# Kernel tuning notes

Hardware: AMD Instinct MI355X
Metric: run time of the kernel (lower is better)

The kernel has to match this reference:

```python
import jax, jax.numpy as jnp
import numpy as np
from jax import lax

WINDOW_SIZE = 11
SIGMA = 1.5
C1 = 0.01 ** 2
C2 = 0.03 ** 2


def _gaussian_window(channels: int) -> jnp.ndarray:
    x = np.arange(WINDOW_SIZE)
    g = np.exp(-((x - WINDOW_SIZE // 2) ** 2) / (2.0 * SIGMA ** 2))
    g = g / g.sum()
    w2d = np.outer(g, g).astype(np.float32)  # [k,k]
    # depthwise kernel: [C, 1, k, k] in OIHW with feature_group_count=C
    return jnp.asarray(np.tile(w2d[None, None], (channels, 1, 1, 1)))


def _depthwise_blur(x: jnp.ndarray, window: jnp.ndarray) -> jnp.ndarray:
    pad = WINDOW_SIZE // 2
    return lax.conv_general_dilated(
        x, window,
        window_strides=(1, 1),
        padding=[(pad, pad), (pad, pad)],
        feature_group_count=x.shape[1],
        dimension_numbers=("NCHW", "OIHW", "NCHW"),
    )


def setup_inputs() -> dict:
    key = jax.random.key(0)
    k1, k2 = jax.random.split(key)
    pred = jax.random.normal(k1, (16, 3, 512, 512), dtype=jnp.float32)
    target = jax.random.normal(k2, (16, 3, 512, 512), dtype=jnp.float32)
    return {"pred": pred, "target": target}


def reference(pred, target):
    pred = (pred + 1.0) / 2.0
    target = (target + 1.0) / 2.0
    channels = pred.shape[1]
    window = _gaussian_window(channels)

    mu_p = _depthwise_blur(pred, window)
    mu_t = _depthwise_blur(target, window)
    mu_p_sq = mu_p * mu_p
    mu_t_sq = mu_t * mu_t
    mu_pt = mu_p * mu_t

    sigma_p_sq = _depthwise_blur(pred * pred, window) - mu_p_sq
    sigma_t_sq = _depthwise_blur(target * target, window) - mu_t_sq
    sigma_pt = _depthwise_blur(pred * target, window) - mu_pt

    ssim_map = ((2.0 * mu_pt + C1) * (2.0 * sigma_pt + C2)) / (
        (mu_p_sq + mu_t_sq + C1) * (sigma_p_sq + sigma_t_sq + C2)
    )
    return 1.0 - jnp.mean(ssim_map)
```

## Files before the change

kernel.cpp:

```cpp
#include <hip/hip_runtime.h>
#include <math.h>


#define IMG 512
#define TW 64
#define TH 16
#define GXD 8
#define GYD 32
#define GZD 48
#define NB (GXD * GYD * GZD)
#define NB4 (NB * 4)
#define VBS 88
#define C1c 0.0001f
#define C2c 0.0009f
#define NTOTAL 12582912.0f
#define WS_NEED (1024 + (size_t)NB4 * 4)

typedef short bf16x8 __attribute__((ext_vector_type(8)));
typedef float f32x4 __attribute__((ext_vector_type(4)));
typedef float f32x2 __attribute__((ext_vector_type(2)));

struct GaussB { unsigned short gb[11]; };

__device__ __forceinline__ unsigned int pkbf(float a, float b) {
    return __builtin_amdgcn_perm(__float_as_uint(b), __float_as_uint(a),
                                 0x07060302u);
}


__device__ __forceinline__ void load_px(const float* __restrict__ pbase,
                                        const float* __restrict__ tbase,
                                        int gx, bool xin, int gy0,
                                        float (&pv)[8], float (&tv)[8]) {
    const bool ok = xin & (gy0 >= 0) & (gy0 <= IMG - 8);
    if (ok) {
        const float* pp = pbase + gy0 * IMG + gx;
        const float* tp = tbase + gy0 * IMG + gx;
        #pragma unroll
        for (int j = 0; j < 8; ++j) {
            pv[j] = pp[j * IMG];
            tv[j] = tp[j * IMG];
        }
    } else {
        #pragma unroll
        for (int j = 0; j < 8; ++j) {
            int gy = gy0 + j;
            bool in = xin && ((unsigned)gy < (unsigned)IMG);
            int idx = in ? (gy * IMG + gx) : 0;
            float a = pbase[idx];
            float b = tbase[idx];
            pv[j] = in ? a : 0.0f;
            tv[j] = in ? b : 0.0f;
        }
    }
}

__device__ __forceinline__ void pass_v_body(
    const float (&pv)[8], const float (&tv)[8], bf16x8 wfrag,
    unsigned short (*vb)[16][VBS], int n16, int vcol) {
    const f32x4 z = {0.0f, 0.0f, 0.0f, 0.0f};
    const f32x2 halfv = {0.5f, 0.5f};
    f32x2 p2[4], t2[4];
    #pragma unroll
    for (int h = 0; h < 4; ++h) {
        f32x2 pr = {pv[2*h], pv[2*h+1]};
        f32x2 tr = {tv[2*h], tv[2*h+1]};
        p2[h] = pr * halfv + halfv;
        t2[h] = tr * halfv + halfv;
    }
    #pragma unroll
    for (int ch = 0; ch < 5; ++ch) {
        union { bf16x8 v; unsigned int u[4]; } f;
        #pragma unroll
        for (int h = 0; h < 4; ++h) {
            f32x2 q;
            if      (ch == 0) q = p2[h];
            else if (ch == 1) q = t2[h];
            else if (ch == 2) q = p2[h] * p2[h];
            else if (ch == 3) q = t2[h] * t2[h];
            else              q = p2[h] * t2[h];
            f.u[h] = pkbf(q.x, q.y);
        }
        f32x4 d = __builtin_amdgcn_mfma_f32_16x16x32_bf16(f.v, wfrag, z, 0, 0, 0);
        union { ushort4 s; unsigned int u[2]; } pk;
        pk.u[0] = pkbf(d[0], d[1]);
        pk.u[1] = pkbf(d[2], d[3]);
        *(ushort4*)&vb[ch][n16][vcol] = pk.s;
    }
}

__device__ __forceinline__ float pass_h_body(
    unsigned short (*vb)[16][VBS], bf16x8 wfrag, int n16, int quad, int w) {
    const f32x4 z = {0.0f, 0.0f, 0.0f, 0.0f};
    float lsum = 0.0f;
    f32x4 r[5];
    #pragma unroll
    for (int ch = 0; ch < 5; ++ch) {
        bf16x8 a = *(const bf16x8*)&vb[ch][n16][16 * w + 8 * quad];
        r[ch] = __builtin_amdgcn_mfma_f32_16x16x32_bf16(a, wfrag, z, 0, 0, 0);
    }
    const f32x2 twov = {2.0f, 2.0f};
    const f32x2 c1v  = {C1c, C1c};
    const f32x2 c2v  = {C2c, C2c};
    #pragma unroll
    for (int jj = 0; jj < 2; ++jj) {
        f32x2 mp  = {r[0][2*jj], r[0][2*jj+1]};
        f32x2 mt  = {r[1][2*jj], r[1][2*jj+1]};
        f32x2 epp = {r[2][2*jj], r[2][2*jj+1]};
        f32x2 ett = {r[3][2*jj], r[3][2*jj+1]};
        f32x2 ept = {r[4][2*jj], r[4][2*jj+1]};
        f32x2 mp2 = mp * mp;
        f32x2 mt2 = mt * mt;
        f32x2 mpt = mp * mt;
        f32x2 sp_ = epp - mp2;
        f32x2 st_ = ett - mt2;
        f32x2 spt = ept - mpt;
        f32x2 num = (mpt * twov + c1v) * (spt * twov + c2v);
        f32x2 den = (mp2 + mt2 + c1v) * (sp_ + st_ + c2v);
        lsum = fmaf(num.x, __builtin_amdgcn_rcpf(den.x), lsum);
        lsum = fmaf(num.y, __builtin_amdgcn_rcpf(den.y), lsum);
    }
    return lsum;
}


__global__ __launch_bounds__(320, 6) void ssim_main_ws(
    const float* __restrict__ pred,
    const float* __restrict__ target,
    const unsigned short* __restrict__ wtab,
    float* __restrict__ partials)
{
    __shared__ unsigned short vb[5][16][VBS];

    const int tid  = threadIdx.x;
    const int w    = tid >> 6;
    const int lane = tid & 63;
    const int quad = lane >> 4;
    const int n16  = lane & 15;
    const int tx0  = blockIdx.x * TW;
    const int ty0  = blockIdx.y * TH;
    const float* __restrict__ pbase = pred   + (size_t)blockIdx.z * (IMG * IMG);
    const float* __restrict__ tbase = target + (size_t)blockIdx.z * (IMG * IMG);

    const int gx   = tx0 - 5 + 16 * w + n16;
    const bool xin = (unsigned)gx < (unsigned)IMG;
    const int gy0  = ty0 - 5 + quad * 8;
    const int vcol = 16 * w + 4 * quad;

    const bf16x8 wfrag = *(const bf16x8*)(wtab + n16 * 32 + quad * 8);

    float pv[8], tv[8];
    load_px(pbase, tbase, gx, xin, gy0, pv, tv);

    pass_v_body(pv, tv, wfrag, vb, n16, vcol);
    __syncthreads();

    float lsum = 0.0f;
    if (w < 4)
        lsum = pass_h_body(vb, wfrag, n16, quad, w);

    #pragma unroll
    for (int off = 32; off > 0; off >>= 1)
        lsum += __shfl_down(lsum, off, 64);
    if (lane == 0 && w < 4) {
        int bid = blockIdx.x + GXD * (blockIdx.y + GYD * blockIdx.z);
        partials[bid * 4 + w] = lsum;
    }
}


__global__ __launch_bounds__(320, 6) void ssim_main_atomic(
    const float* __restrict__ pred,
    const float* __restrict__ target,
    float* __restrict__ sink,
    GaussB gwb)
{
    __shared__ unsigned short Wmat[16][32];
    __shared__ unsigned short vb[5][16][VBS];
    __shared__ float red[5];

    const int tid  = threadIdx.x;
    const int w    = tid >> 6;
    const int lane = tid & 63;
    const int quad = lane >> 4;
    const int n16  = lane & 15;
    const int tx0  = blockIdx.x * TW;
    const int ty0  = blockIdx.y * TH;
    const float* __restrict__ pbase = pred   + (size_t)blockIdx.z * (IMG * IMG);
    const float* __restrict__ tbase = target + (size_t)blockIdx.z * (IMG * IMG);

    const int gx   = tx0 - 5 + 16 * w + n16;
    const bool xin = (unsigned)gx < (unsigned)IMG;
    const int gy0  = ty0 - 5 + quad * 8;
    const int vcol = 16 * w + 4 * quad;

    float pv[8], tv[8];
    load_px(pbase, tbase, gx, xin, gy0, pv, tv);

    for (int idx = tid; idx < 512; idx += 320) {
        int i = idx >> 5, k = idx & 31, d = k - i;
        Wmat[i][k] = (d >= 0 && d <= 10) ? gwb.gb[d] : 0;
    }
    __syncthreads();
    const bf16x8 wfrag = *(const bf16x8*)&Wmat[n16][quad * 8];

    pass_v_body(pv, tv, wfrag, vb, n16, vcol);
    __syncthreads();

    float lsum = 0.0f;
    if (w < 4)
        lsum = pass_h_body(vb, wfrag, n16, quad, w);

    #pragma unroll
    for (int off = 32; off > 0; off >>= 1)
        lsum += __shfl_down(lsum, off, 64);
    if (lane == 0) red[w] = lsum;
    __syncthreads();
    if (tid == 0)
        atomicAdd(sink, red[0] + red[1] + red[2] + red[3]);
}


__global__ __launch_bounds__(1024) void ssim_reduce(const float* __restrict__ partials,
                                                    float* __restrict__ out)
{
    __shared__ float red[16];
    const int tid = threadIdx.x;
    float s = 0.0f;
    const float4* p4 = (const float4*)partials;
    #pragma unroll
    for (int j = 0; j < NB4 / 4096; ++j) {
        float4 v = p4[tid + 1024 * j];
        s += v.x + v.y + v.z + v.w;
    }
    #pragma unroll
    for (int off = 32; off > 0; off >>= 1)
        s += __shfl_down(s, off, 64);
    if ((tid & 63) == 0) red[tid >> 6] = s;
    __syncthreads();
    if (tid == 0) {
        float t = 0.0f;
        #pragma unroll
        for (int k = 0; k < 16; ++k) t += red[k];
        out[0] = 1.0f - t / NTOTAL;
    }
}

__global__ void ssim_zero(float* accum) { accum[0] = 0.0f; }
__global__ void ssim_final(const float* accum, float* out) {
    out[0] = 1.0f - accum[0] / NTOTAL;
}


static unsigned short g_hostW[512];

extern "C" void kernel_launch(void* const* d_in, const int* in_sizes, int n_in,
                              void* d_out, int out_size, void* d_ws, size_t ws_size,
                              hipStream_t stream) {
    const float* pred   = (const float*)d_in[0];
    const float* target = (const float*)d_in[1];
    float* out = (float*)d_out;

    GaussB gwb;
    double vals[11], s = 0.0;
    for (int i = 0; i < 11; ++i) {
        double d = (double)i - 5.0;
        vals[i] = exp(-(d * d) / (2.0 * 1.5 * 1.5));
        s += vals[i];
    }
    for (int i = 0; i < 11; ++i) {
        float f = (float)(vals[i] / s);
        unsigned int u;
        __builtin_memcpy(&u, &f, 4);
        unsigned int rounded = (u + 0x7FFFu + ((u >> 16) & 1u)) >> 16;
        gwb.gb[i] = (unsigned short)rounded;
    }
    for (int i = 0; i < 16; ++i)
        for (int k = 0; k < 32; ++k) {
            int d = k - i;
            g_hostW[i * 32 + k] = (d >= 0 && d <= 10) ? gwb.gb[d] : 0;
        }

    dim3 grid(GXD, GYD, GZD);
    if (ws_size >= WS_NEED) {
        unsigned short* wtab = (unsigned short*)d_ws;
        float* partials = (float*)((char*)d_ws + 1024);
        hipMemcpyAsync(wtab, g_hostW, sizeof(g_hostW),
                       hipMemcpyHostToDevice, stream);
        ssim_main_ws<<<grid, 320, 0, stream>>>(pred, target, wtab, partials);
        ssim_reduce<<<1, 1024, 0, stream>>>(partials, out);
    } else {
        float* accum = (float*)d_ws;
        ssim_zero<<<1, 1, 0, stream>>>(accum);
        ssim_main_atomic<<<grid, 320, 0, stream>>>(pred, target, accum, gwb);
        ssim_final<<<1, 1, 0, stream>>>(accum, out);
    }
}
```

Baseline: 137.6 us.

## Shrink tiles to single-wave 16x16 blocks and build weight table on device

Each block is now one 64-thread wave covering a 16x16 output tile, loading two 16-column halo strips per lane instead of five waves covering a 64x16 tile. This removes idle waves in the horizontal pass and the cross-wave reduction, and gives many more small blocks. The cost is more halo reloading per output (26 columns loaded per 16 outputs, versus 80 per 64) and four times as many blocks. The host-to-device memcpy of the weight table is replaced with a tiny init kernel.

```diff
diff --git a/kernel.cpp b/kernel.cpp
--- a/kernel.cpp
+++ b/kernel.cpp
@@ -3,18 +3,15 @@
 
 
 #define IMG 512
-#define TW 64
-#define TH 16
-#define GXD 8
+#define GXD 32
 #define GYD 32
 #define GZD 48
 #define NB (GXD * GYD * GZD)
-#define NB4 (NB * 4)
-#define VBS 88
+#define VBS 40
 #define C1c 0.0001f
 #define C2c 0.0009f
 #define NTOTAL 12582912.0f
-#define WS_NEED (1024 + (size_t)NB4 * 4)
+#define WS_NEED (1024 + (size_t)NB * 4)
 
 typedef short bf16x8 __attribute__((ext_vector_type(8)));
 typedef float f32x4 __attribute__((ext_vector_type(4)));
@@ -90,13 +87,13 @@
 }
 
 __device__ __forceinline__ float pass_h_body(
-    unsigned short (*vb)[16][VBS], bf16x8 wfrag, int n16, int quad, int w) {
+    unsigned short (*vb)[16][VBS], bf16x8 wfrag, int n16, int quad) {
     const f32x4 z = {0.0f, 0.0f, 0.0f, 0.0f};
     float lsum = 0.0f;
     f32x4 r[5];
     #pragma unroll
     for (int ch = 0; ch < 5; ++ch) {
-        bf16x8 a = *(const bf16x8*)&vb[ch][n16][16 * w + 8 * quad];
+        bf16x8 a = *(const bf16x8*)&vb[ch][n16][8 * quad];
         r[ch] = __builtin_amdgcn_mfma_f32_16x16x32_bf16(a, wfrag, z, 0, 0, 0);
     }
     const f32x2 twov = {2.0f, 2.0f};
@@ -124,7 +121,7 @@
 }
 
 
-__global__ __launch_bounds__(320, 6) void ssim_main_ws(
+__global__ __launch_bounds__(64, 6) void ssim_main_ws(
     const float* __restrict__ pred,
     const float* __restrict__ target,
     const unsigned short* __restrict__ wtab,
@@ -132,44 +129,47 @@
 {
     __shared__ unsigned short vb[5][16][VBS];
 
-    const int tid  = threadIdx.x;
-    const int w    = tid >> 6;
-    const int lane = tid & 63;
+    const int lane = threadIdx.x;
     const int quad = lane >> 4;
     const int n16  = lane & 15;
-    const int tx0  = blockIdx.x * TW;
-    const int ty0  = blockIdx.y * TH;
+    const int c0   = blockIdx.x * 16;
+    const int ty0  = blockIdx.y * 16;
     const float* __restrict__ pbase = pred   + (size_t)blockIdx.z * (IMG * IMG);
     const float* __restrict__ tbase = target + (size_t)blockIdx.z * (IMG * IMG);
 
-    const int gx   = tx0 - 5 + 16 * w + n16;
-    const bool xin = (unsigned)gx < (unsigned)IMG;
-    const int gy0  = ty0 - 5 + quad * 8;
-    const int vcol = 16 * w + 4 * quad;
+    const int gy0 = ty0 - 5 + quad * 8;
+    const int gxA = c0 - 5 + n16;
+    const int gxB = c0 + 11 + n16;
 
     const bf16x8 wfrag = *(const bf16x8*)(wtab + n16 * 32 + quad * 8);
 
-    float pv[8], tv[8];
-    load_px(pbase, tbase, gx, xin, gy0, pv, tv);
-
-    pass_v_body(pv, tv, wfrag, vb, n16, vcol);
-    __syncthreads();
-
-    float lsum = 0.0f;
-    if (w < 4)
-        lsum = pass_h_body(vb, wfrag, n16, quad, w);
+    float pvA[8], tvA[8], pvB[8], tvB[8];
+    load_px(pbase, tbase, gxA, (unsigned)gxA < (unsigned)IMG, gy0, pvA, tvA);
+    load_px(pbase, tbase, gxB, (unsigned)gxB < (unsigned)IMG, gy0, pvB, tvB);
+
+    pass_v_body(pvA, tvA, wfrag, vb, n16, 4 * quad);
+    pass_v_body(pvB, tvB, wfrag, vb, n16, 16 + 4 * quad);
+    __syncthreads();
+
+    float lsum = pass_h_body(vb, wfrag, n16, quad);
 
     #pragma unroll
     for (int off = 32; off > 0; off >>= 1)
         lsum += __shfl_down(lsum, off, 64);
-    if (lane == 0 && w < 4) {
+    if (lane == 0) {
         int bid = blockIdx.x + GXD * (blockIdx.y + GYD * blockIdx.z);
-        partials[bid * 4 + w] = lsum;
-    }
-}
-
-
-__global__ __launch_bounds__(320, 6) void ssim_main_atomic(
+        partials[bid] = lsum;
+    }
+}
+
+__global__ void ssim_winit(unsigned short* __restrict__ wtab, GaussB gwb) {
+    int idx = threadIdx.x;
+    int i = idx >> 5, k = idx & 31, d = k - i;
+    wtab[idx] = (d >= 0 && d <= 10) ? gwb.gb[d] : 0;
+}
+
+
+__global__ __launch_bounds__(64, 6) void ssim_main_atomic(
     const float* __restrict__ pred,
     const float* __restrict__ target,
     float* __restrict__ sink,
@@ -177,47 +177,43 @@
 {
     __shared__ unsigned short Wmat[16][32];
     __shared__ unsigned short vb[5][16][VBS];
-    __shared__ float red[5];
-
-    const int tid  = threadIdx.x;
-    const int w    = tid >> 6;
-    const int lane = tid & 63;
+
+    const int lane = threadIdx.x;
     const int quad = lane >> 4;
     const int n16  = lane & 15;
-    const int tx0  = blockIdx.x * TW;
-    const int ty0  = blockIdx.y * TH;
+    const int c0   = blockIdx.x * 16;
+    const int ty0  = blockIdx.y * 16;
     const float* __restrict__ pbase = pred   + (size_t)blockIdx.z * (IMG * IMG);
     const float* __restrict__ tbase = target + (size_t)blockIdx.z * (IMG * IMG);
 
-    const int gx   = tx0 - 5 + 16 * w + n16;
-    const bool xin = (unsigned)gx < (unsigned)IMG;
-    const int gy0  = ty0 - 5 + quad * 8;
-    const int vcol = 16 * w + 4 * quad;
-
-    float pv[8], tv[8];
-    load_px(pbase, tbase, gx, xin, gy0, pv, tv);
-
-    for (int idx = tid; idx < 512; idx += 320) {
+    const int gy0 = ty0 - 5 + quad * 8;
+    const int gxA = c0 - 5 + n16;
+    const int gxB = c0 + 11 + n16;
+
+    float pvA[8], tvA[8], pvB[8], tvB[8];
+    load_px(pbase, tbase, gxA, (unsigned)gxA < (unsigned)IMG, gy0, pvA, tvA);
+    load_px(pbase, tbase, gxB, (unsigned)gxB < (unsigned)IMG, gy0, pvB, tvB);
+
+    #pragma unroll
+    for (int r = 0; r < 8; ++r) {
+        int idx = lane + 64 * r;
         int i = idx >> 5, k = idx & 31, d = k - i;
         Wmat[i][k] = (d >= 0 && d <= 10) ? gwb.gb[d] : 0;
     }
     __syncthreads();
     const bf16x8 wfrag = *(const bf16x8*)&Wmat[n16][quad * 8];
 
-    pass_v_body(pv, tv, wfrag, vb, n16, vcol);
-    __syncthreads();
-
-    float lsum = 0.0f;
-    if (w < 4)
-        lsum = pass_h_body(vb, wfrag, n16, quad, w);
+    pass_v_body(pvA, tvA, wfrag, vb, n16, 4 * quad);
+    pass_v_body(pvB, tvB, wfrag, vb, n16, 16 + 4 * quad);
+    __syncthreads();
+
+    float lsum = pass_h_body(vb, wfrag, n16, quad);
 
     #pragma unroll
     for (int off = 32; off > 0; off >>= 1)
         lsum += __shfl_down(lsum, off, 64);
-    if (lane == 0) red[w] = lsum;
-    __syncthreads();
-    if (tid == 0)
-        atomicAdd(sink, red[0] + red[1] + red[2] + red[3]);
+    if (lane == 0)
+        atomicAdd(sink, lsum);
 }
 
 
@@ -229,7 +225,7 @@
     float s = 0.0f;
     const float4* p4 = (const float4*)partials;
     #pragma unroll
-    for (int j = 0; j < NB4 / 4096; ++j) {
+    for (int j = 0; j < NB / 4096; ++j) {
         float4 v = p4[tid + 1024 * j];
         s += v.x + v.y + v.z + v.w;
     }
@@ -251,8 +247,6 @@
     out[0] = 1.0f - accum[0] / NTOTAL;
 }
 
-
-static unsigned short g_hostW[512];
 
 extern "C" void kernel_launch(void* const* d_in, const int* in_sizes, int n_in,
                               void* d_out, int out_size, void* d_ws, size_t ws_size,
@@ -275,24 +269,18 @@
         unsigned int rounded = (u + 0x7FFFu + ((u >> 16) & 1u)) >> 16;
         gwb.gb[i] = (unsigned short)rounded;
     }
-    for (int i = 0; i < 16; ++i)
-        for (int k = 0; k < 32; ++k) {
-            int d = k - i;
-            g_hostW[i * 32 + k] = (d >= 0 && d <= 10) ? gwb.gb[d] : 0;
-        }
 
     dim3 grid(GXD, GYD, GZD);
     if (ws_size >= WS_NEED) {
         unsigned short* wtab = (unsigned short*)d_ws;
         float* partials = (float*)((char*)d_ws + 1024);
-        hipMemcpyAsync(wtab, g_hostW, sizeof(g_hostW),
-                       hipMemcpyHostToDevice, stream);
-        ssim_main_ws<<<grid, 320, 0, stream>>>(pred, target, wtab, partials);
+        ssim_winit<<<1, 512, 0, stream>>>(wtab, gwb);
+        ssim_main_ws<<<grid, 64, 0, stream>>>(pred, target, wtab, partials);
         ssim_reduce<<<1, 1024, 0, stream>>>(partials, out);
     } else {
         float* accum = (float*)d_ws;
         ssim_zero<<<1, 1, 0, stream>>>(accum);
-        ssim_main_atomic<<<grid, 320, 0, stream>>>(pred, target, accum, gwb);
+        ssim_main_atomic<<<grid, 64, 0, stream>>>(pred, target, accum, gwb);
         ssim_final<<<1, 1, 0, stream>>>(accum, out);
     }
 }
```

New measurement: 170.2 us. +23.7%, slower.

## Stage input tiles through LDS with float4 loads and build weights on device

Applied to the files above, without the earlier changes.

Each block now loads its 32x84 haloed input tile for pred and target cooperatively with coalesced float4 global loads into shared memory. Threads then read their 8-row column strips from LDS instead of issuing scalar strided global loads, and the same buffer is reused for the vertical-pass output. The host-to-device memcpy of the banded weight matrix is replaced by a tiny init kernel. The cost is a larger LDS footprint (about 22 KB per block, which may limit occupancy) and an extra barrier.

```diff
diff --git a/kernel.cpp b/kernel.cpp
--- a/kernel.cpp
+++ b/kernel.cpp
@@ -11,6 +11,9 @@
 #define NB (GXD * GYD * GZD)
 #define NB4 (NB * 4)
 #define VBS 88
+#define SROW 86
+#define NF4 21
+#define NF4TOT (32 * NF4)
 #define C1c 0.0001f
 #define C2c 0.0009f
 #define NTOTAL 12582912.0f
@@ -28,32 +31,30 @@
 }
 
 
-__device__ __forceinline__ void load_px(const float* __restrict__ pbase,
-                                        const float* __restrict__ tbase,
-                                        int gx, bool xin, int gy0,
-                                        float (&pv)[8], float (&tv)[8]) {
-    const bool ok = xin & (gy0 >= 0) & (gy0 <= IMG - 8);
-    if (ok) {
-        const float* pp = pbase + gy0 * IMG + gx;
-        const float* tp = tbase + gy0 * IMG + gx;
-        #pragma unroll
-        for (int j = 0; j < 8; ++j) {
-            pv[j] = pp[j * IMG];
-            tv[j] = tp[j * IMG];
+__device__ __forceinline__ float4 ldf4(const float* __restrict__ base,
+                                       int gy, int gx0) {
+    float4 v = make_float4(0.f, 0.f, 0.f, 0.f);
+    if ((unsigned)gy < (unsigned)IMG) {
+        if ((unsigned)gx0 <= (unsigned)(IMG - 4)) {
+            v = *(const float4*)(base + gy * IMG + gx0);
+        } else {
+            float* e = (float*)&v;
+            #pragma unroll
+            for (int k = 0; k < 4; ++k) {
+                int gx = gx0 + k;
+                if ((unsigned)gx < (unsigned)IMG) e[k] = base[gy * IMG + gx];
+            }
         }
-    } else {
-        #pragma unroll
-        for (int j = 0; j < 8; ++j) {
-            int gy = gy0 + j;
-            bool in = xin && ((unsigned)gy < (unsigned)IMG);
-            int idx = in ? (gy * IMG + gx) : 0;
-            float a = pbase[idx];
-            float b = tbase[idx];
-            pv[j] = in ? a : 0.0f;
-            tv[j] = in ? b : 0.0f;
-        }
-    }
-}
+    }
+    return v;
+}
+
+__device__ __forceinline__ void stw(float* arr, int r, int c4, float4 v) {
+    float* p = arr + r * SROW + 4 * c4;
+    *(float2*)p       = make_float2(v.x, v.y);
+    *(float2*)(p + 2) = make_float2(v.z, v.w);
+}
+
 
 __device__ __forceinline__ void pass_v_body(
     const float (&pv)[8], const float (&tv)[8], bf16x8 wfrag,
@@ -130,7 +131,10 @@
     const unsigned short* __restrict__ wtab,
     float* __restrict__ partials)
 {
-    __shared__ unsigned short vb[5][16][VBS];
+    __shared__ float sbuf[2 * 32 * SROW];
+    float* ps = sbuf;
+    float* ts = sbuf + 32 * SROW;
+    auto vb = reinterpret_cast<unsigned short (*)[16][VBS]>(sbuf);
 
     const int tid  = threadIdx.x;
     const int w    = tid >> 6;
@@ -142,17 +146,34 @@
     const float* __restrict__ pbase = pred   + (size_t)blockIdx.z * (IMG * IMG);
     const float* __restrict__ tbase = target + (size_t)blockIdx.z * (IMG * IMG);
 
-    const int gx   = tx0 - 5 + 16 * w + n16;
-    const bool xin = (unsigned)gx < (unsigned)IMG;
-    const int gy0  = ty0 - 5 + quad * 8;
-    const int vcol = 16 * w + 4 * quad;
-
     const bf16x8 wfrag = *(const bf16x8*)(wtab + n16 * 32 + quad * 8);
 
+    for (int id = tid; id < NF4TOT; id += 320) {
+        const int r  = id / NF4;
+        const int c4 = id - r * NF4;
+        const int gy  = ty0 - 5 + r;
+        const int gx0 = tx0 - 8 + 4 * c4;
+        float4 pvv = ldf4(pbase, gy, gx0);
+        float4 tvv = ldf4(tbase, gy, gx0);
+        stw(ps, r, c4, pvv);
+        stw(ts, r, c4, tvv);
+    }
+    __syncthreads();
+
+    const int col = 3 + 16 * w + n16;
     float pv[8], tv[8];
-    load_px(pbase, tbase, gx, xin, gy0, pv, tv);
-
-    pass_v_body(pv, tv, wfrag, vb, n16, vcol);
+    {
+        const float* pc = ps + (quad * 8) * SROW + col;
+        const float* tc = ts + (quad * 8) * SROW + col;
+        #pragma unroll
+        for (int j = 0; j < 8; ++j) {
+            pv[j] = pc[j * SROW];
+            tv[j] = tc[j * SROW];
+        }
+    }
+    __syncthreads();
+
+    pass_v_body(pv, tv, wfrag, vb, n16, 16 * w + 4 * quad);
     __syncthreads();
 
     float lsum = 0.0f;
@@ -166,6 +187,12 @@
         int bid = blockIdx.x + GXD * (blockIdx.y + GYD * blockIdx.z);
         partials[bid * 4 + w] = lsum;
     }
+}
+
+__global__ void ssim_winit(unsigned short* __restrict__ wtab, GaussB gwb) {
+    int idx = threadIdx.x;
+    int i = idx >> 5, k = idx & 31, d = k - i;
+    wtab[idx] = (d >= 0 && d <= 10) ? gwb.gb[d] : 0;
 }
 
 
@@ -175,9 +202,12 @@
     float* __restrict__ sink,
     GaussB gwb)
 {
+    __shared__ float sbuf[2 * 32 * SROW];
     __shared__ unsigned short Wmat[16][32];
-    __shared__ unsigned short vb[5][16][VBS];
     __shared__ float red[5];
+    float* ps = sbuf;
+    float* ts = sbuf + 32 * SROW;
+    auto vb = reinterpret_cast<unsigned short (*)[16][VBS]>(sbuf);
 
     const int tid  = threadIdx.x;
     const int w    = tid >> 6;
@@ -189,22 +219,38 @@
     const float* __restrict__ pbase = pred   + (size_t)blockIdx.z * (IMG * IMG);
     const float* __restrict__ tbase = target + (size_t)blockIdx.z * (IMG * IMG);
 
-    const int gx   = tx0 - 5 + 16 * w + n16;
-    const bool xin = (unsigned)gx < (unsigned)IMG;
-    const int gy0  = ty0 - 5 + quad * 8;
-    const int vcol = 16 * w + 4 * quad;
-
-    float pv[8], tv[8];
-    load_px(pbase, tbase, gx, xin, gy0, pv, tv);
-
     for (int idx = tid; idx < 512; idx += 320) {
         int i = idx >> 5, k = idx & 31, d = k - i;
         Wmat[i][k] = (d >= 0 && d <= 10) ? gwb.gb[d] : 0;
     }
+
+    for (int id = tid; id < NF4TOT; id += 320) {
+        const int r  = id / NF4;
+        const int c4 = id - r * NF4;
+        const int gy  = ty0 - 5 + r;
+        const int gx0 = tx0 - 8 + 4 * c4;
+        float4 pvv = ldf4(pbase, gy, gx0);
+        float4 tvv = ldf4(tbase, gy, gx0);
+        stw(ps, r, c4, pvv);
+        stw(ts, r, c4, tvv);
+    }
     __syncthreads();
     const bf16x8 wfrag = *(const bf16x8*)&Wmat[n16][quad * 8];
 
-    pass_v_body(pv, tv, wfrag, vb, n16, vcol);
+    const int col = 3 + 16 * w + n16;
+    float pv[8], tv[8];
+    {
+        const float* pc = ps + (quad * 8) * SROW + col;
+        const float* tc = ts + (quad * 8) * SROW + col;
+        #pragma unroll
+        for (int j = 0; j < 8; ++j) {
+            pv[j] = pc[j * SROW];
+            tv[j] = tc[j * SROW];
+        }
+    }
+    __syncthreads();
+
+    pass_v_body(pv, tv, wfrag, vb, n16, 16 * w + 4 * quad);
     __syncthreads();
 
     float lsum = 0.0f;
@@ -252,8 +298,6 @@
 }
 
 
-static unsigned short g_hostW[512];
-
 extern "C" void kernel_launch(void* const* d_in, const int* in_sizes, int n_in,
                               void* d_out, int out_size, void* d_ws, size_t ws_size,
                               hipStream_t stream) {
@@ -275,18 +319,12 @@
         unsigned int rounded = (u + 0x7FFFu + ((u >> 16) & 1u)) >> 16;
         gwb.gb[i] = (unsigned short)rounded;
     }
-    for (int i = 0; i < 16; ++i)
-        for (int k = 0; k < 32; ++k) {
-            int d = k - i;
-            g_hostW[i * 32 + k] = (d >= 0 && d <= 10) ? gwb.gb[d] : 0;
-        }
 
     dim3 grid(GXD, GYD, GZD);
     if (ws_size >= WS_NEED) {
         unsigned short* wtab = (unsigned short*)d_ws;
         float* partials = (float*)((char*)d_ws + 1024);
-        hipMemcpyAsync(wtab, g_hostW, sizeof(g_hostW),
-                       hipMemcpyHostToDevice, stream);
+        ssim_winit<<<1, 512, 0, stream>>>(wtab, gwb);
         ssim_main_ws<<<grid, 320, 0, stream>>>(pred, target, wtab, partials);
         ssim_reduce<<<1, 1024, 0, stream>>>(partials, out);
     } else {
```

After: 149.8 us. 8.9% more time.

## Process two row strips per block and build weight table on device

Applied to the files above, without the earlier changes.

Each block now covers 32 rows instead of 16, loading both strips up front and running the vertical and horizontal passes twice with light LDS barriers between them. This halves the grid and the per-block setup cost and lets the second strip's global loads overlap the first strip's compute. The occupancy hint rises to 8 blocks per CU, while the extra live registers for the second strip may strain that target. The host-to-device memcpy of the weight table is replaced by a tiny init kernel.

```diff
diff --git a/kernel.cpp b/kernel.cpp
--- a/kernel.cpp
+++ b/kernel.cpp
@@ -4,9 +4,9 @@
 
 #define IMG 512
 #define TW 64
-#define TH 16
+#define TH 32
 #define GXD 8
-#define GYD 32
+#define GYD 16
 #define GZD 48
 #define NB (GXD * GYD * GZD)
 #define NB4 (NB * 4)
@@ -15,6 +15,12 @@
 #define C2c 0.0009f
 #define NTOTAL 12582912.0f
 #define WS_NEED (1024 + (size_t)NB4 * 4)
+
+#define LGKM_BAR() do {                                            \
+    asm volatile("s_waitcnt lgkmcnt(0)" ::: "memory");             \
+    __builtin_amdgcn_s_barrier();                                  \
+    asm volatile("" ::: "memory");                                 \
+} while (0)
 
 typedef short bf16x8 __attribute__((ext_vector_type(8)));
 typedef float f32x4 __attribute__((ext_vector_type(4)));
@@ -124,7 +130,7 @@
 }
 
 
-__global__ __launch_bounds__(320, 6) void ssim_main_ws(
+__global__ __launch_bounds__(320, 8) void ssim_main_ws(
     const float* __restrict__ pred,
     const float* __restrict__ target,
     const unsigned short* __restrict__ wtab,
@@ -144,20 +150,27 @@
 
     const int gx   = tx0 - 5 + 16 * w + n16;
     const bool xin = (unsigned)gx < (unsigned)IMG;
-    const int gy0  = ty0 - 5 + quad * 8;
+    const int gy0a = ty0 - 5 + quad * 8;
+    const int gy0b = ty0 + 11 + quad * 8;
     const int vcol = 16 * w + 4 * quad;
 
     const bf16x8 wfrag = *(const bf16x8*)(wtab + n16 * 32 + quad * 8);
 
-    float pv[8], tv[8];
-    load_px(pbase, tbase, gx, xin, gy0, pv, tv);
-
-    pass_v_body(pv, tv, wfrag, vb, n16, vcol);
-    __syncthreads();
-
+    float pv0[8], tv0[8], pv1[8], tv1[8];
+    load_px(pbase, tbase, gx, xin, gy0a, pv0, tv0);
+    load_px(pbase, tbase, gx, xin, gy0b, pv1, tv1);
+
+    pass_v_body(pv0, tv0, wfrag, vb, n16, vcol);
+    LGKM_BAR();
     float lsum = 0.0f;
     if (w < 4)
         lsum = pass_h_body(vb, wfrag, n16, quad, w);
+    LGKM_BAR();
+
+    pass_v_body(pv1, tv1, wfrag, vb, n16, vcol);
+    LGKM_BAR();
+    if (w < 4)
+        lsum += pass_h_body(vb, wfrag, n16, quad, w);
 
     #pragma unroll
     for (int off = 32; off > 0; off >>= 1)
@@ -168,8 +181,14 @@
     }
 }
 
-
-__global__ __launch_bounds__(320, 6) void ssim_main_atomic(
+__global__ void ssim_winit(unsigned short* __restrict__ wtab, GaussB gwb) {
+    int idx = threadIdx.x;
+    int i = idx >> 5, k = idx & 31, d = k - i;
+    wtab[idx] = (d >= 0 && d <= 10) ? gwb.gb[d] : 0;
+}
+
+
+__global__ __launch_bounds__(320, 8) void ssim_main_atomic(
     const float* __restrict__ pred,
     const float* __restrict__ target,
     float* __restrict__ sink,
@@ -191,11 +210,13 @@
 
     const int gx   = tx0 - 5 + 16 * w + n16;
     const bool xin = (unsigned)gx < (unsigned)IMG;
-    const int gy0  = ty0 - 5 + quad * 8;
+    const int gy0a = ty0 - 5 + quad * 8;
+    const int gy0b = ty0 + 11 + quad * 8;
     const int vcol = 16 * w + 4 * quad;
 
-    float pv[8], tv[8];
-    load_px(pbase, tbase, gx, xin, gy0, pv, tv);
+    float pv0[8], tv0[8], pv1[8], tv1[8];
+    load_px(pbase, tbase, gx, xin, gy0a, pv0, tv0);
+    load_px(pbase, tbase, gx, xin, gy0b, pv1, tv1);
 
     for (int idx = tid; idx < 512; idx += 320) {
         int i = idx >> 5, k = idx & 31, d = k - i;
@@ -204,12 +225,16 @@
     __syncthreads();
     const bf16x8 wfrag = *(const bf16x8*)&Wmat[n16][quad * 8];
 
-    pass_v_body(pv, tv, wfrag, vb, n16, vcol);
-    __syncthreads();
-
+    pass_v_body(pv0, tv0, wfrag, vb, n16, vcol);
+    __syncthreads();
     float lsum = 0.0f;
     if (w < 4)
         lsum = pass_h_body(vb, wfrag, n16, quad, w);
+    __syncthreads();
+    pass_v_body(pv1, tv1, wfrag, vb, n16, vcol);
+    __syncthreads();
+    if (w < 4)
+        lsum += pass_h_body(vb, wfrag, n16, quad, w);
 
     #pragma unroll
     for (int off = 32; off > 0; off >>= 1)
@@ -252,8 +277,6 @@
 }
 
 
-static unsigned short g_hostW[512];
-
 extern "C" void kernel_launch(void* const* d_in, const int* in_sizes, int n_in,
                               void* d_out, int out_size, void* d_ws, size_t ws_size,
                               hipStream_t stream) {
@@ -275,18 +298,12 @@
         unsigned int rounded = (u + 0x7FFFu + ((u >> 16) & 1u)) >> 16;
         gwb.gb[i] = (unsigned short)rounded;
     }
-    for (int i = 0; i < 16; ++i)
-        for (int k = 0; k < 32; ++k) {
-            int d = k - i;
-            g_hostW[i * 32 + k] = (d >= 0 && d <= 10) ? gwb.gb[d] : 0;
-        }
 
     dim3 grid(GXD, GYD, GZD);
     if (ws_size >= WS_NEED) {
         unsigned short* wtab = (unsigned short*)d_ws;
         float* partials = (float*)((char*)d_ws + 1024);
-        hipMemcpyAsync(wtab, g_hostW, sizeof(g_hostW),
-                       hipMemcpyHostToDevice, stream);
+        ssim_winit<<<1, 512, 0, stream>>>(wtab, gwb);
         ssim_main_ws<<<grid, 320, 0, stream>>>(pred, target, wtab, partials);
         ssim_reduce<<<1, 1024, 0, stream>>>(partials, out);
     } else {
```

Result: no change. 138.7 us (+0.8%).
